# Optimization experiments

Measured on AMD Instinct MI355X. Metric: run time of the kernel, lower is better.

The kernel has to match this reference:

```python
import jax, jax.numpy as jnp
import numpy as np

B, L, D_MODEL, D_FF, N_EXPERTS, TOP_K = 32, 256, 512, 2048, 8, 2
EPS = 1e-9


def setup_inputs() -> dict:
    key = jax.random.key(0)
    ks = jax.random.split(key, 7)
    scale1 = 1.0 / np.sqrt(D_MODEL)
    scale2 = 1.0 / np.sqrt(D_FF)
    return {
        "cycle_curve_data": jax.random.normal(ks[0], (B, L, D_MODEL), jnp.float32),
        "logits": jax.random.normal(ks[1], (B, N_EXPERTS), jnp.float32),
        "moe_masks": jax.random.randint(ks[2], (B, N_EXPERTS), 0, 2, jnp.int32),
        "W1": jax.random.normal(ks[3], (N_EXPERTS, D_MODEL, D_FF), jnp.float32) * scale1,
        "b1": jax.random.normal(ks[4], (N_EXPERTS, D_FF), jnp.float32) * scale1,
        "W2": jax.random.normal(ks[5], (N_EXPERTS, D_FF, D_MODEL), jnp.float32) * scale2,
        "b2": jax.random.normal(ks[6], (N_EXPERTS, D_MODEL), jnp.float32) * scale2,
    }


def _gates(logits, moe_masks):
    # softmax over experts, zero out unavailable experts, keep top-k, renormalize
    mask = (moe_masks == 1).astype(logits.dtype)               # [B, E]
    p = jax.nn.softmax(logits, axis=1) * mask                  # [B, E]
    _, idx = jax.lax.top_k(p, TOP_K)                           # [B, K]
    topk_mask = jnp.zeros_like(p).at[jnp.arange(p.shape[0])[:, None], idx].set(1.0)
    p = p * topk_mask
    return p / (jnp.sum(p, axis=1, keepdims=True) + EPS)       # [B, E]


def reference(cycle_curve_data, logits, moe_masks, W1, b1, W2, b2):
    gates = _gates(logits, moe_masks)                          # [B, E]
    x = cycle_curve_data                                       # [B, L, D]
    # dense equivalent of per-expert gather -> MLP -> gate-weighted scatter-combine
    h = jnp.einsum("bld,edf->eblf", x, W1) + b1[:, None, None, :]   # [E,B,L,F]
    h = jax.nn.gelu(h, approximate=False)
    out = jnp.einsum("be,eblf,efd->bld", gates, h, W2)
    out = out + jnp.einsum("be,ed->bd", gates, b2)[:, None, :]      # [B,L,D]
    return out
```

## Files before the change

kernel.cpp:

```cpp
#include <hip/hip_runtime.h>

#define B_SZ 32
#define L_SZ 256
#define D_SZ 512
#define F_SZ 2048
#define E_SZ 8
#define P_SZ 64
#define BK2  32

typedef __attribute__((ext_vector_type(8)))  short bf16x8;
typedef __attribute__((ext_vector_type(16))) float f32x16;

__device__ __forceinline__ unsigned short f2bf(float f) {
  unsigned int u = __builtin_bit_cast(unsigned int, f);
  u += 0x7fffu + ((u >> 16) & 1u);
  return (unsigned short)(u >> 16);
}

__device__ __forceinline__ void async16(const void* g, void* l) {
  __builtin_amdgcn_global_load_lds(
      (const __attribute__((address_space(1))) unsigned int*)g,
      (__attribute__((address_space(3))) unsigned int*)l, 16, 0, 0);
}

__device__ __forceinline__ float gelu_f(float x) {
  float a = fabsf(x) * 0.70710678118654752f;
  float t = __builtin_amdgcn_rcpf(1.0f + 0.3275911f * a);
  float y = t * (0.254829592f +
            t * (-0.284496736f +
            t * (1.421413741f +
            t * (-1.453152027f +
            t * 1.061405429f))));
  float e = __expf(-a * a);
  float erf_abs = 1.0f - y * e;
  float erf_v = (x < 0.f) ? -erf_abs : erf_abs;
  return 0.5f * x * (1.0f + erf_v);
}

template <int NT>
__device__ __forceinline__ void transpose_tile(
    const float* __restrict__ ip, unsigned short* __restrict__ op,
    int R, int C, int r0, int c0, float* tile, int tid) {
  int tx = tid & 63, ty = tid >> 6;
  constexpr int RY = NT / 64;
#pragma unroll
  for (int i = 0; i < 64 / RY; ++i) {
    int r = i * RY + ty;
    tile[r * 65 + tx] = ip[(size_t)(r0 + r) * C + c0 + tx];
  }
  __syncthreads();
#pragma unroll
  for (int uu = 0; uu < 1024 / NT; ++uu) {
    int u = uu * NT + tid;
    int cc = u >> 4, q = u & 15;
    ushort4 o;
    o.x = f2bf(tile[(q * 4 + 0) * 65 + cc]);
    o.y = f2bf(tile[(q * 4 + 1) * 65 + cc]);
    o.z = f2bf(tile[(q * 4 + 2) * 65 + cc]);
    o.w = f2bf(tile[(q * 4 + 3) * 65 + cc]);
    *(ushort4*)(op + (size_t)(c0 + cc) * R + r0 + q * 4) = o;
  }
}

#define PREP_CONV_BLKS 4096
#define PREP_TR_BLKS   2048
#define PREP_TOTAL     (1 + PREP_CONV_BLKS + PREP_TR_BLKS)

__global__ __launch_bounds__(256) void prep_kernel(
    const float* __restrict__ logits, const int* __restrict__ masks,
    const float* __restrict__ x,
    const float* __restrict__ W1,
    int* __restrict__ sel_e, float* __restrict__ sel_g,
    unsigned short* __restrict__ xb,
    unsigned short* __restrict__ w1t) {
  __shared__ float tile[64 * 65];
  int blk = blockIdx.x;
  int tid = threadIdx.x;

  if (blk == 0) {
    int b = tid;
    if (b >= B_SZ) return;
    float lg[E_SZ], p[E_SZ];
    float mx = -1e30f;
    for (int e = 0; e < E_SZ; ++e) { lg[e] = logits[b * E_SZ + e]; mx = fmaxf(mx, lg[e]); }
    float s = 0.f;
    for (int e = 0; e < E_SZ; ++e) { p[e] = expf(lg[e] - mx); s += p[e]; }
    for (int e = 0; e < E_SZ; ++e) p[e] = (masks[b * E_SZ + e] == 1) ? (p[e] / s) : 0.f;
    int i0 = 0, i1 = 1; float v0 = -1.f, v1 = -1.f;
    for (int e = 0; e < E_SZ; ++e) {
      float v = p[e];
      if (v > v0)      { v1 = v0; i1 = i0; v0 = v; i0 = e; }
      else if (v > v1) { v1 = v;  i1 = e; }
    }
    float den = v0 + v1 + 1e-9f;
    sel_e[2 * b] = i0;  sel_e[2 * b + 1] = i1;
    sel_g[2 * b] = v0 / den;
    sel_g[2 * b + 1] = v1 / den;
    return;
  }
  blk -= 1;

  if (blk < PREP_CONV_BLKS) {
    int i = blk * 256 + tid;
    float4 v = ((const float4*)x)[i];
    ushort4 o;
    o.x = f2bf(v.x); o.y = f2bf(v.y); o.z = f2bf(v.z); o.w = f2bf(v.w);
    ((ushort4*)xb)[i] = o;
    return;
  }
  blk -= PREP_CONV_BLKS;

  int z = blk >> 8;
  int rem = blk & 255;
  int tr = rem >> 5, tc = rem & 31;
  transpose_tile<256>(W1 + (size_t)z * D_SZ * F_SZ, w1t + (size_t)z * D_SZ * F_SZ,
                      D_SZ, F_SZ, tr * 64, tc * 64, tile, tid);
}

__global__ __launch_bounds__(512, 4) void moe_gemm1(
    const unsigned short* __restrict__ Xb,
    const unsigned short* __restrict__ W1t,
    const float* __restrict__ b1,
    const int* __restrict__ sel_e,
    unsigned short* __restrict__ H,
    const float* __restrict__ W2,
    unsigned short* __restrict__ w2t) {
  __shared__ __align__(16) char smem[49152];
  int tid = threadIdx.x;
  int lin = blockIdx.x;

  if (lin >= 1024) {
    int blk = lin - 1024;
    int z = blk >> 8;
    int rem = blk & 255;
    int tr = rem >> 3, tc = rem & 7;
    transpose_tile<512>(W2 + (size_t)z * F_SZ * D_SZ, w2t + (size_t)z * F_SZ * D_SZ,
                        F_SZ, D_SZ, tr * 64, tc * 64, (float*)smem, tid);
    return;
  }

  unsigned short* As = (unsigned short*)smem;
  unsigned short* Bs = (unsigned short*)(smem + 16384);

  int f  = lin & 7;
  int l0 = ((lin >> 3) & 1) * 128;
  int p  = lin >> 4;
  int f0 = f * 256;
  int b  = p >> 1;
  int e  = sel_e[p];

  int lane = tid & 63;
  int w = tid >> 6;
  int wm = w & 1, wn = w >> 1;
  int m32 = lane & 31, kh = lane >> 5;
  int sw = (m32 >> 1) & 3;

  const unsigned short* Abase = Xb  + ((size_t)b * L_SZ + l0) * D_SZ;
  const unsigned short* Bbase = W1t + ((size_t)e * F_SZ + f0) * D_SZ;

  int sa   = tid;
  int rowa = sa >> 2,  ka  = ((sa  & 3) ^ ((rowa >> 1) & 3)) * 8;
  int sb1  = tid + 512;
  int rowb = sb1 >> 2, kb1 = ((sb1 & 3) ^ ((rowb >> 1) & 3)) * 8;

  const size_t aoffA  = (size_t)rowa * D_SZ + ka;
  const size_t aoffB1 = (size_t)rowb * D_SZ + kb1;

  f32x16 acc[2][2] = {};

#define G1_COMPUTE(CB)                                                       \
  _Pragma("unroll")                                                          \
  for (int s = 0; s < 2; ++s) {                                              \
    int ko = ((((s << 1) | kh) ^ sw) << 3);                                  \
    bf16x8 a0  = *(const bf16x8*)&As[(CB) * 4096 + (wm * 64 +      m32) * BK2 + ko]; \
    bf16x8 a1  = *(const bf16x8*)&As[(CB) * 4096 + (wm * 64 + 32 + m32) * BK2 + ko]; \
    bf16x8 b0  = *(const bf16x8*)&Bs[(CB) * 8192 + (wn * 64 +      m32) * BK2 + ko]; \
    bf16x8 b1f = *(const bf16x8*)&Bs[(CB) * 8192 + (wn * 64 + 32 + m32) * BK2 + ko]; \
    acc[0][0] = __builtin_amdgcn_mfma_f32_32x32x16_bf16(a0, b0,  acc[0][0], 0, 0, 0); \
    acc[0][1] = __builtin_amdgcn_mfma_f32_32x32x16_bf16(a0, b1f, acc[0][1], 0, 0, 0); \
    acc[1][0] = __builtin_amdgcn_mfma_f32_32x32x16_bf16(a1, b0,  acc[1][0], 0, 0, 0); \
    acc[1][1] = __builtin_amdgcn_mfma_f32_32x32x16_bf16(a1, b1f, acc[1][1], 0, 0, 0); \
  }

  async16(Abase + aoffA,  &As[sa * 8]);
  async16(Bbase + aoffA,  &Bs[sa * 8]);
  async16(Bbase + aoffB1, &Bs[sb1 * 8]);
  __syncthreads();

#pragma unroll 2
  for (int t = 0; t < 15; ++t) {
    int cb = t & 1, nb = cb ^ 1;
    int kk = (t + 1) * BK2;
    async16(Abase + aoffA  + kk, &As[nb * 4096 + sa * 8]);
    async16(Bbase + aoffA  + kk, &Bs[nb * 8192 + sa * 8]);
    async16(Bbase + aoffB1 + kk, &Bs[nb * 8192 + sb1 * 8]);
    G1_COMPUTE(cb)
    __syncthreads();
  }
  G1_COMPUTE(1)
#undef G1_COMPUTE

  float b1v[2];
#pragma unroll
  for (int tj = 0; tj < 2; ++tj)
    b1v[tj] = b1[e * F_SZ + f0 + wn * 64 + tj * 32 + m32];

  unsigned short* Hp = H + ((size_t)p * L_SZ + l0) * F_SZ + f0;
#pragma unroll
  for (int ti = 0; ti < 2; ++ti)
#pragma unroll
    for (int tj = 0; tj < 2; ++tj) {
      int col = wn * 64 + tj * 32 + m32;
#pragma unroll
      for (int r = 0; r < 16; ++r) {
        int row = wm * 64 + ti * 32 + (r & 3) + 8 * (r >> 2) + 4 * kh;
        Hp[(size_t)row * F_SZ + col] = f2bf(gelu_f(acc[ti][tj][r] + b1v[tj]));
      }
    }
}

__global__ __launch_bounds__(128, 2) void moe_gemm2(
    const unsigned short* __restrict__ H,
    const unsigned short* __restrict__ W2t,
    const float* __restrict__ b2,
    const int* __restrict__ sel_e,
    const float* __restrict__ sel_g,
    float* __restrict__ part,
    float* __restrict__ Out) {
  __shared__ __align__(16) unsigned short As[2][128 * BK2];
  __shared__ __align__(16) unsigned short Bs[2][64 * BK2];

  int lin = blockIdx.x;
  int q   = lin & 7;
  int d   = (lin >> 3) & 7;
  int g8  = lin >> 6;
  int gg  = g8 * 8 + q;
  int p   = gg >> 1;
  int l0  = (gg & 1) * 128;
  int d0  = d * 64;
  int b   = p >> 1;
  int e   = sel_e[p];
  float g = sel_g[p];

  int tid = threadIdx.x;
  int lane = tid & 63;
  int wm = tid >> 6;
  int m32 = lane & 31, kh = lane >> 5;
  int sw = (m32 >> 1) & 3;

  const unsigned short* Abase = H   + ((size_t)p * L_SZ + l0) * F_SZ;
  const unsigned short* Bbase = W2t + ((size_t)e * D_SZ + d0) * F_SZ;

  int    saA[4]; size_t aoffA[4];
#pragma unroll
  for (int j = 0; j < 4; ++j) {
    int s = tid + j * 128;
    int row = s >> 2, ks = ((s & 3) ^ ((row >> 1) & 3)) * 8;
    saA[j] = s; aoffA[j] = (size_t)row * F_SZ + ks;
  }
  int    saB[2]; size_t aoffB[2];
#pragma unroll
  for (int j = 0; j < 2; ++j) {
    int s = tid + j * 128;
    int row = s >> 2, ks = ((s & 3) ^ ((row >> 1) & 3)) * 8;
    saB[j] = s; aoffB[j] = (size_t)row * F_SZ + ks;
  }

  f32x16 acc[2][2] = {};

#define G2_COMPUTE(CB)                                                       \
  _Pragma("unroll")                                                          \
  for (int s = 0; s < 2; ++s) {                            \
    int ko = (((s << 1) | kh) ^ sw) << 3;                                    \
    bf16x8 a0  = *(const bf16x8*)&As[CB][(wm * 64 +      m32) * BK2 + ko];   \
    bf16x8 a1  = *(const bf16x8*)&As[CB][(wm * 64 + 32 + m32) * BK2 + ko];   \
    bf16x8 b0  = *(const bf16x8*)&Bs[CB][(          m32) * BK2 + ko];        \
    bf16x8 b1f = *(const bf16x8*)&Bs[CB][(     32 + m32) * BK2 + ko];        \
    acc[0][0] = __builtin_amdgcn_mfma_f32_32x32x16_bf16(a0, b0,  acc[0][0], 0, 0, 0); \
    acc[0][1] = __builtin_amdgcn_mfma_f32_32x32x16_bf16(a0, b1f, acc[0][1], 0, 0, 0); \
    acc[1][0] = __builtin_amdgcn_mfma_f32_32x32x16_bf16(a1, b0,  acc[1][0], 0, 0, 0); \
    acc[1][1] = __builtin_amdgcn_mfma_f32_32x32x16_bf16(a1, b1f, acc[1][1], 0, 0, 0); \
  }

#pragma unroll
  for (int j = 0; j < 4; ++j) async16(Abase + aoffA[j], &As[0][saA[j] * 8]);
#pragma unroll
  for (int j = 0; j < 2; ++j) async16(Bbase + aoffB[j], &Bs[0][saB[j] * 8]);
  __syncthreads();

#pragma unroll 2
  for (int t = 0; t < 63; ++t) {
    int cb = t & 1, nb = cb ^ 1;
    int kk = (t + 1) * BK2;
#pragma unroll
    for (int j = 0; j < 4; ++j)
      async16(Abase + aoffA[j] + kk, &As[nb][saA[j] * 8]);
#pragma unroll
    for (int j = 0; j < 2; ++j)
      async16(Bbase + aoffB[j] + kk, &Bs[nb][saB[j] * 8]);
    G2_COMPUTE(cb)
    __syncthreads();
  }
  G2_COMPUTE(1)
#undef G2_COMPUTE

  float bias[2] = {0.f, 0.f};
  if (p & 1) {
    int e0 = sel_e[2 * b], e1 = sel_e[2 * b + 1];
    float g0 = sel_g[2 * b], g1 = sel_g[2 * b + 1];
#pragma unroll
    for (int tj = 0; tj < 2; ++tj) {
      int dd = d0 + tj * 32 + m32;
      bias[tj] = g0 * b2[e0 * D_SZ + dd] + g1 * b2[e1 * D_SZ + dd];
    }
  }
  float* dst = (p & 1) ? Out : part;
  float* Op = dst + ((size_t)b * L_SZ + l0) * D_SZ + d0;
#pragma unroll
  for (int ti = 0; ti < 2; ++ti)
#pragma unroll
    for (int tj = 0; tj < 2; ++tj) {
      int col = tj * 32 + m32;
#pragma unroll
      for (int r = 0; r < 16; ++r) {
        int row = wm * 64 + ti * 32 + (r & 3) + 8 * (r >> 2) + 4 * kh;
        Op[(size_t)row * D_SZ + col] = g * acc[ti][tj][r] + bias[tj];
      }
    }
}

__global__ __launch_bounds__(256) void combine_kernel(
    const float* __restrict__ part, float* __restrict__ Out) {
  int i = blockIdx.x * 256 + threadIdx.x;
  float4 pv = ((const float4*)part)[i];
  float4 o  = ((float4*)Out)[i];
  o.x += pv.x; o.y += pv.y; o.z += pv.z; o.w += pv.w;
  ((float4*)Out)[i] = o;
}

extern "C" void kernel_launch(void* const* d_in, const int* in_sizes, int n_in,
                              void* d_out, int out_size, void* d_ws, size_t ws_size,
                              hipStream_t stream) {
  const float* x      = (const float*)d_in[0];
  const float* logits = (const float*)d_in[1];
  const int*   masks  = (const int*)d_in[2];
  const float* W1     = (const float*)d_in[3];
  const float* b1     = (const float*)d_in[4];
  const float* W2     = (const float*)d_in[5];
  const float* b2     = (const float*)d_in[6];
  float* out = (float*)d_out;

  char* ws = (char*)d_ws;
  int*   sel_e = (int*)ws;
  float* sel_g = (float*)(ws + 256);
  unsigned short* xb  = (unsigned short*)(ws + 1024);
  unsigned short* w1t = xb  + (size_t)B_SZ * L_SZ * D_SZ;
  unsigned short* w2t = w1t + (size_t)E_SZ * F_SZ * D_SZ;
  unsigned short* Hbuf = w2t + (size_t)E_SZ * D_SZ * F_SZ;
  float* part = (float*)(ws + 1024);

  prep_kernel<<<PREP_TOTAL, 256, 0, stream>>>(logits, masks, x, W1,
                                              sel_e, sel_g, xb, w1t);
  moe_gemm1<<<3072, 512, 0, stream>>>(xb, w1t, b1, sel_e, Hbuf, W2, w2t);
  moe_gemm2<<<1024, 128, 0, stream>>>(Hbuf, w2t, b2, sel_e, sel_g, part, out);
  combine_kernel<<<(B_SZ * L_SZ * D_SZ / 4) / 256, 256, 0, stream>>>(part, out);
}
```

Baseline: 259.2 us.

## Keep two async tile loads in flight with explicit vmcnt waits in both GEMMs

Both GEMM main loops now issue the loads for the next two K-tiles before computing. Each iteration uses explicit s_waitcnt vmcnt counts and raw barriers in place of __syncthreads, which drained every outstanding load. The intent is to overlap global-to-LDS transfers with MFMA work more deeply within the same double buffer. The cost is an extra barrier per iteration, and correctness now depends on exact vmcnt accounting and the compiler fences.

```diff
diff --git a/kernel.cpp b/kernel.cpp
--- a/kernel.cpp
+++ b/kernel.cpp
@@ -10,6 +10,10 @@
 
 typedef __attribute__((ext_vector_type(8)))  short bf16x8;
 typedef __attribute__((ext_vector_type(16))) float f32x16;
+
+#define VMCNT(N) asm volatile("s_waitcnt vmcnt(" #N ")" ::: "memory")
+#define CFENCE() asm volatile("" ::: "memory")
+#define SBAR()   __builtin_amdgcn_s_barrier()
 
 __device__ __forceinline__ unsigned short f2bf(float f) {
   unsigned int u = __builtin_bit_cast(unsigned int, f);
@@ -168,6 +172,13 @@
 
   f32x16 acc[2][2] = {};
 
+#define G1_STAGE(T, NB) do {                                                 \
+    int kk = (T) * BK2;                                                      \
+    async16(Abase + aoffA  + kk, &As[(NB) * 4096 + sa * 8]);                 \
+    async16(Bbase + aoffA  + kk, &Bs[(NB) * 8192 + sa * 8]);                 \
+    async16(Bbase + aoffB1 + kk, &Bs[(NB) * 8192 + sb1 * 8]);                \
+  } while (0)
+
 #define G1_COMPUTE(CB)                                                       \
   _Pragma("unroll")                                                          \
   for (int s = 0; s < 2; ++s) {                                              \
@@ -182,23 +193,26 @@
     acc[1][1] = __builtin_amdgcn_mfma_f32_32x32x16_bf16(a1, b1f, acc[1][1], 0, 0, 0); \
   }
 
-  async16(Abase + aoffA,  &As[sa * 8]);
-  async16(Bbase + aoffA,  &Bs[sa * 8]);
-  async16(Bbase + aoffB1, &Bs[sb1 * 8]);
-  __syncthreads();
+  G1_STAGE(0, 0);
+  G1_STAGE(1, 1);
+  VMCNT(3);
+  SBAR(); CFENCE();
 
 #pragma unroll 2
-  for (int t = 0; t < 15; ++t) {
-    int cb = t & 1, nb = cb ^ 1;
-    int kk = (t + 1) * BK2;
-    async16(Abase + aoffA  + kk, &As[nb * 4096 + sa * 8]);
-    async16(Bbase + aoffA  + kk, &Bs[nb * 8192 + sa * 8]);
-    async16(Bbase + aoffB1 + kk, &Bs[nb * 8192 + sb1 * 8]);
+  for (int t = 0; t < 14; ++t) {
+    int cb = t & 1;
     G1_COMPUTE(cb)
-    __syncthreads();
-  }
+    CFENCE(); SBAR(); CFENCE();
+    G1_STAGE(t + 2, cb);
+    VMCNT(3);
+    SBAR(); CFENCE();
+  }
+  G1_COMPUTE(0)
+  VMCNT(0);
+  SBAR(); CFENCE();
   G1_COMPUTE(1)
 #undef G1_COMPUTE
+#undef G1_STAGE
 
   float b1v[2];
 #pragma unroll
@@ -267,6 +281,16 @@
   }
 
   f32x16 acc[2][2] = {};
+
+#define G2_STAGE(T, NB) do {                                                 \
+    int kk = (T) * BK2;                                                      \
+    _Pragma("unroll")                                                        \
+    for (int j = 0; j < 4; ++j)                                              \
+      async16(Abase + aoffA[j] + kk, &As[NB][saA[j] * 8]);                   \
+    _Pragma("unroll")                                                        \
+    for (int j = 0; j < 2; ++j)                                              \
+      async16(Bbase + aoffB[j] + kk, &Bs[NB][saB[j] * 8]);                   \
+  } while (0)
 
 #define G2_COMPUTE(CB)                                                       \
   _Pragma("unroll")                                                          \
@@ -282,27 +306,26 @@
     acc[1][1] = __builtin_amdgcn_mfma_f32_32x32x16_bf16(a1, b1f, acc[1][1], 0, 0, 0); \
   }
 
-#pragma unroll
-  for (int j = 0; j < 4; ++j) async16(Abase + aoffA[j], &As[0][saA[j] * 8]);
-#pragma unroll
-  for (int j = 0; j < 2; ++j) async16(Bbase + aoffB[j], &Bs[0][saB[j] * 8]);
-  __syncthreads();
+  G2_STAGE(0, 0);
+  G2_STAGE(1, 1);
+  VMCNT(6);
+  SBAR(); CFENCE();
 
 #pragma unroll 2
-  for (int t = 0; t < 63; ++t) {
-    int cb = t & 1, nb = cb ^ 1;
-    int kk = (t + 1) * BK2;
-#pragma unroll
-    for (int j = 0; j < 4; ++j)
-      async16(Abase + aoffA[j] + kk, &As[nb][saA[j] * 8]);
-#pragma unroll
-    for (int j = 0; j < 2; ++j)
-      async16(Bbase + aoffB[j] + kk, &Bs[nb][saB[j] * 8]);
+  for (int t = 0; t < 62; ++t) {
+    int cb = t & 1;
     G2_COMPUTE(cb)
-    __syncthreads();
-  }
+    CFENCE(); SBAR(); CFENCE();
+    G2_STAGE(t + 2, cb);
+    VMCNT(6);
+    SBAR(); CFENCE();
+  }
+  G2_COMPUTE(0)
+  VMCNT(0);
+  SBAR(); CFENCE();
   G2_COMPUTE(1)
 #undef G2_COMPUTE
+#undef G2_STAGE
 
   float bias[2] = {0.f, 0.f};
   if (p & 1) {
```

After: 239.7 us. 7.5% less time.
